# Kernel tuning notes

Hardware: AMD Instinct MI355X
Metric: run time of the kernel (lower is better)

## Reference

```python
import jax, jax.numpy as jnp
import numpy as np

R, N, B, S = 20, 4096, 16, 256          # relations, total nodes, graphs, nodes per graph
DIN, HID, H = 512, 128, 4               # in_dim, hidden_dim, num_heads
D = HID * H                              # flattened node-feature width (=512)
E = 16384                                # edges per relation
NEG_SLOPE = 0.2


def _gat(h, src, dst, W, al, ar, b):
    # DGL GATConv, eval mode (dropout off), identity residual (in == H*out), allow_zero_in_degree
    z = (h @ W).reshape(N, H, HID)                        # [N,H,Dh]
    el = (z * al).sum(-1)                                 # [N,H]
    er = (z * ar).sum(-1)                                 # [N,H]
    e = jax.nn.leaky_relu(el[src] + er[dst], NEG_SLOPE)   # [E,H]
    m = jax.ops.segment_max(e, dst, num_segments=N)       # per-dst max (edge softmax)
    ex = jnp.exp(e - m[dst])
    den = jax.ops.segment_sum(ex, dst, num_segments=N)
    alpha = ex / den[dst]                                 # [E,H]
    agg = jax.ops.segment_sum(alpha[..., None] * z[src], dst, num_segments=N)
    return agg + h.reshape(N, H, HID) + b, alpha


def _rgat_conv(h, src, dst, W, al, ar, b):
    # HeteroGraphConv with aggregate='mean' over R relations; scan keeps memory flat
    def body(acc, xs):
        s, d, Wr, alr, arr, br = xs
        out, alpha = _gat(h, s, d, Wr, alr, arr, br)
        return acc + out, alpha.mean(-1)                  # attention meaned over heads -> [E]
    acc, attn = jax.lax.scan(body, jnp.zeros((N, H, HID), h.dtype), (src, dst, W, al, ar, b))
    return acc / R, attn                                  # [N,H,Dh], [R,E]


def setup_inputs() -> dict:
    key = jax.random.key(0)
    ks = jax.random.split(key, 24)
    f32 = jnp.float32
    p = lambda k, shape: jax.random.normal(k, shape, f32) * 0.05
    z = lambda shape: jnp.zeros(shape, f32)
    return {
        'feat': jax.random.normal(ks[0], (N, DIN), f32),
        'hyp_emb': jax.random.normal(ks[1], (B, D), f32),
        'edge_src': jax.random.randint(ks[2], (R, E), 0, N),
        'edge_dst': jax.random.randint(ks[3], (R, E), 0, N),
        'W1': p(ks[4], (R, DIN, H * HID)), 'al1': p(ks[5], (R, H, HID)), 'ar1': p(ks[6], (R, H, HID)), 'b1': z((R, H, HID)),
        'W2': p(ks[7], (R, D, H * HID)), 'al2': p(ks[8], (R, H, HID)), 'ar2': p(ks[9], (R, H, HID)), 'b2': z((R, H, HID)),
        'Wq': p(ks[10], (D, D)), 'bq': z(D), 'Wk': p(ks[11], (D, D)), 'bk': z(D),
        'Wv': p(ks[12], (D, D)), 'bv': z(D), 'Wo': p(ks[13], (D, D)), 'bo': z(D),
        'Wn1': p(ks[14], (2 * D, HID)), 'bn1': z(HID), 'Wn2': p(ks[15], (HID, 2)), 'bn2': z(2),
    }


def reference(feat, hyp_emb, edge_src, edge_dst,
              W1, al1, ar1, b1, W2, al2, ar2, b2,
              Wq, bq, Wk, bk, Wv, bv, Wo, bo, Wn1, bn1, Wn2, bn2):
    # --- RGAT (rgat_generation) layer 1 + attention weights ---
    h1, attn = _rgat_conv(feat, edge_src, edge_dst, W1, al1, ar1, b1)
    h1 = jax.nn.elu(h1.reshape(N, D))
    # --- layer 2 ---
    h2, _ = _rgat_conv(h1, edge_src, edge_dst, W2, al2, ar2, b2)
    feats = h2.reshape(N, D)
    # --- node importance: scatter-add edge attention onto dst nodes, summed over etypes ---
    imp = jax.ops.segment_sum(attn.reshape(-1), edge_dst.reshape(-1), num_segments=N)
    feats_p = feats.reshape(B, S, D)                      # uniform graphs: split+pad == reshape
    weighted = feats_p * imp.reshape(B, S)[..., None]
    # --- MultiheadAttention(embed=D, heads=4): query = hyp_emb broadcast to all S positions ---
    Hm, Dm = 4, D // 4
    q = (hyp_emb @ Wq + bq).reshape(B, Hm, 1, Dm)         # identical query at every position
    k = (feats_p @ Wk + bk).reshape(B, S, Hm, Dm).transpose(0, 2, 1, 3)
    v = (feats_p @ Wv + bv).reshape(B, S, Hm, Dm).transpose(0, 2, 1, 3)
    scores = jnp.einsum('bhqd,bhkd->bhqk', q, k) / jnp.sqrt(jnp.float32(Dm))
    a = jax.nn.softmax(scores, axis=-1)                   # [B,Hm,1,S]
    ctx = jnp.einsum('bhqk,bhkd->bhqd', a, v).reshape(B, 1, D)
    attn_out = jnp.broadcast_to(ctx @ Wo + bo, (B, S, D))
    # --- node classifier on concat(weighted feats, attention output) ---
    combined = jnp.concatenate([weighted, attn_out], axis=-1).reshape(N, 2 * D)
    node_logits = jax.nn.relu(combined @ Wn1 + bn1) @ Wn2 + bn2
    return node_logits, attn
```

## Files before the change

kernel.cpp:

```cpp
#include <hip/hip_runtime.h>
#include <hip/hip_bf16.h>
#include <math.h>

#define NREL 20
#define NN   4096
#define NE   16384
#define DF   512
#define NHD  4
#define DHH  128
#define NB   16
#define NS   256

typedef __attribute__((ext_vector_type(8))) __bf16 bf16x8;
typedef __attribute__((ext_vector_type(4))) float f32x4;
typedef __attribute__((ext_vector_type(2))) float f32x2;

struct f8 { unsigned char b; };

__device__ inline float bf2f(unsigned short u) {
    union { float f; unsigned int i; } c; c.i = ((unsigned int)u) << 16; return c.f;
}
__device__ inline unsigned short f2bu(float f) {
    union { __hip_bfloat16 b; unsigned short u; } c; c.b = __float2bfloat16(f); return c.u;
}
__device__ inline void storeOut(float* p, float v) { *p = v; }
__device__ inline void storeOut(__hip_bfloat16* p, float v) { *p = __float2bfloat16(v); }

__device__ inline void load_lds16(const __hip_bfloat16* g, __hip_bfloat16* l) {
    __builtin_amdgcn_global_load_lds(
        (const __attribute__((address_space(1))) unsigned int*)(const void*)g,
        (__attribute__((address_space(3))) unsigned int*)(void*)l, 16, 0, 0);
}

__device__ inline int kswz(int f, int row) { return f ^ (((row) & 7) << 3); }

__global__ __launch_bounds__(256) void prep_kernel(
    const float* __restrict__ feat, unsigned short* __restrict__ featbf,
    const float* __restrict__ b1, const float* __restrict__ b2,
    const float* __restrict__ bk, const float* __restrict__ bv,
    float* __restrict__ bsum1, float* __restrict__ bsum2,
    float* __restrict__ bkv, int* __restrict__ cnt, float* __restrict__ imp)
{
    int blk = blockIdx.x, t = threadIdx.x;
    if (blk < 1024) {
        int idx = blk * 256 + t;
        int row = idx >> 6;
        int f = (idx & 63) * 8;
        int fs = kswz(f, row);
        const float4* ip = (const float4*)&feat[(size_t)row * DF + f];
        float4 v0 = ip[0], v1 = ip[1];
        union { unsigned short u[8]; uint4 q; } o;
        o.u[0] = f2bu(v0.x); o.u[1] = f2bu(v0.y); o.u[2] = f2bu(v0.z); o.u[3] = f2bu(v0.w);
        o.u[4] = f2bu(v1.x); o.u[5] = f2bu(v1.y); o.u[6] = f2bu(v1.z); o.u[7] = f2bu(v1.w);
        *(uint4*)(featbf + (size_t)row * DF + fs) = o.q;
    } else if (blk == 1024) {
        #pragma unroll
        for (int rep = 0; rep < 2; ++rep) {
            int f = t + rep * 256;
            float s1 = 0.f, s2 = 0.f;
            #pragma unroll
            for (int r = 0; r < NREL; ++r) { s1 += b1[r * DF + f]; s2 += b2[r * DF + f]; }
            bsum1[f] = s1; bsum2[f] = s2;
        }
        for (int i = t; i < NN; i += 256) imp[i] = 0.f;
    } else if (blk == 1025) {
        #pragma unroll
        for (int j = 0; j < 4; ++j) {
            int f = t + j * 256;
            bkv[f] = (f < DF) ? bk[f] : bv[f - DF];
        }
    } else {
        int idx = (blk - 1026) * 256 + t;
        cnt[idx] = 0;
    }
}

__global__ void count_kernel(const int* __restrict__ dst, int* __restrict__ cnt) {
    int idx = blockIdx.x * 256 + threadIdx.x;
    int r = idx / NE;
    atomicAdd(&cnt[r * NN + dst[idx]], 1);
}

__global__ void scan_kernel(const int* __restrict__ cnt, int* __restrict__ rowptr,
                            int* __restrict__ woff, int* __restrict__ rowptr2,
                            int* __restrict__ croff) {
    int r = blockIdx.x;
    int t = threadIdx.x;
    __shared__ int sums[1024];
    int v[4]; int local = 0;
    if (r < NREL) {
        #pragma unroll
        for (int j = 0; j < 4; ++j) { v[j] = cnt[r * NN + t * 4 + j]; local += v[j]; }
    } else {
        #pragma unroll
        for (int j = 0; j < 4; ++j) {
            int s = 0;
            for (int rel = 0; rel < NREL; ++rel) {
                croff[rel * NN + t * 4 + j] = s;
                s += cnt[rel * NN + t * 4 + j];
            }
            v[j] = s; local += s;
        }
    }
    sums[t] = local;
    __syncthreads();
    for (int off = 1; off < 1024; off <<= 1) {
        int x = (t >= off) ? sums[t - off] : 0;
        __syncthreads();
        sums[t] += x;
        __syncthreads();
    }
    int run = (t == 0) ? 0 : sums[t - 1];
    if (r < NREL) {
        #pragma unroll
        for (int j = 0; j < 4; ++j) {
            rowptr[r * (NN + 1) + t * 4 + j] = run;
            woff[r * NN + t * 4 + j] = run;
            run += v[j];
        }
        if (t == 1023) rowptr[r * (NN + 1) + NN] = run;
    } else {
        #pragma unroll
        for (int j = 0; j < 4; ++j) { rowptr2[t * 4 + j] = run; run += v[j]; }
        if (t == 1023) rowptr2[NN] = run;
    }
}

__global__ void fill_kernel(const int* __restrict__ dst, const int* __restrict__ src,
                            int* __restrict__ woff, int* __restrict__ srcCSR,
                            int* __restrict__ eidCSR) {
    int idx = blockIdx.x * 256 + threadIdx.x;
    int r = idx / NE; int e = idx % NE;
    int pos = atomicAdd(&woff[r * NN + dst[idx]], 1);
    srcCSR[r * NE + pos] = src[idx];
    eidCSR[r * NE + pos] = e;
}

__global__ __launch_bounds__(256) void transw_kernel(
    const float* __restrict__ W, __hip_bfloat16* __restrict__ Wt, int K, int N)
{
    int r = blockIdx.z;
    __shared__ float t[32][33];
    int k0 = blockIdx.x * 32, n0 = blockIdx.y * 32;
    int tx = threadIdx.x % 32, ty = threadIdx.x / 32;
    #pragma unroll
    for (int kk = ty; kk < 32; kk += 8)
        t[kk][tx] = W[((size_t)r * K + k0 + kk) * N + n0 + tx];
    __syncthreads();
    #pragma unroll
    for (int nn = ty; nn < 32; nn += 8) {
        int row = n0 + nn;
        Wt[((size_t)r * N + row) * K + kswz(k0 + tx, row)] = __float2bfloat16(t[tx][nn]);
    }
}

__global__ __launch_bounds__(256) void transw2_kernel(
    const float* __restrict__ W1, const float* __restrict__ W2,
    const float* __restrict__ Wk, const float* __restrict__ Wv,
    __hip_bfloat16* __restrict__ Wt1, __hip_bfloat16* __restrict__ Wt2,
    __hip_bfloat16* __restrict__ WtKV)
{
    int z = blockIdx.z;
    const float* Wsrc; __hip_bfloat16* Wdst;
    if (z < NREL)           { Wsrc = W1 + (size_t)z * DF * DF;          Wdst = Wt1 + (size_t)z * DF * DF; }
    else if (z < 2 * NREL)  { Wsrc = W2 + (size_t)(z - NREL) * DF * DF; Wdst = Wt2 + (size_t)(z - NREL) * DF * DF; }
    else if (z == 2 * NREL) { Wsrc = Wk;                                Wdst = WtKV; }
    else                    { Wsrc = Wv;                                Wdst = WtKV + (size_t)DF * DF; }
    __shared__ float t[32][33];
    int k0 = blockIdx.x * 32, n0 = blockIdx.y * 32;
    int tx = threadIdx.x % 32, ty = threadIdx.x / 32;
    #pragma unroll
    for (int kk = ty; kk < 32; kk += 8)
        t[kk][tx] = Wsrc[(size_t)(k0 + kk) * DF + n0 + tx];
    __syncthreads();
    #pragma unroll
    for (int nn = ty; nn < 32; nn += 8) {
        int row = n0 + nn;
        Wdst[(size_t)row * DF + kswz(k0 + tx, row)] = __float2bfloat16(t[tx][nn]);
    }
}

__global__ __launch_bounds__(512) void zgemm8(
    const __hip_bfloat16* __restrict__ A,
    const __hip_bfloat16* __restrict__ BtAll,
    unsigned char* __restrict__ Zall,
    const float* __restrict__ al, const float* __restrict__ ar,
    float* __restrict__ el, float* __restrict__ er)
{
    const int r = blockIdx.z;
    const __hip_bfloat16* Bt = BtAll + (size_t)r * DF * DF;
    unsigned char* Z = Zall + (size_t)r * NN * DF;
    const int rowBase = blockIdx.y * 256;
    const int colBase = blockIdx.x * 256;
    __shared__ __hip_bfloat16 As[2][256][64];
    __shared__ __hip_bfloat16 Bs[2][256][64];
    const int tid = threadIdx.x;
    const int w = tid >> 6, l = tid & 63;
    const int wr = w >> 2, wc = w & 3;
    const int m15 = l & 15, q = l >> 4;
    const int swr = m15 & 7;

    const __hip_bfloat16* Ag = A + (size_t)(rowBase + (tid >> 3)) * DF + (tid & 7) * 8;
    const __hip_bfloat16* Bg = Bt + (size_t)(colBase + (tid >> 3)) * DF + (tid & 7) * 8;
    __hip_bfloat16* AsT = &As[0][0][0] + tid * 8;
    __hip_bfloat16* BsT = &Bs[0][0][0] + tid * 8;

#define STAGE_A(buf, half, kt) do { \
        const __hip_bfloat16* s_ = Ag + (size_t)((half) * 128) * DF + (kt) * 64; \
        __hip_bfloat16* d_ = AsT + (buf) * 16384 + (half) * 8192; \
        load_lds16(s_, d_); \
        load_lds16(s_ + (size_t)64 * DF, d_ + 4096); } while (0)
#define STAGE_B(buf, half, kt) do { \
        const __hip_bfloat16* s_ = Bg + (size_t)((half) * 128) * DF + (kt) * 64; \
        __hip_bfloat16* d_ = BsT + (buf) * 16384 + (half) * 8192; \
        load_lds16(s_, d_); \
        load_lds16(s_ + (size_t)64 * DF, d_ + 4096); } while (0)

    f32x4 acc[8][4];
    #pragma unroll
    for (int i = 0; i < 8; ++i)
        #pragma unroll
        for (int j = 0; j < 4; ++j) acc[i][j] = (f32x4){0.f, 0.f, 0.f, 0.f};

    const int NT = DF / 64;
    STAGE_A(0, 0, 0); STAGE_A(0, 1, 0); STAGE_B(0, 0, 0); STAGE_B(0, 1, 0);
    STAGE_A(1, 0, 1); STAGE_A(1, 1, 1); STAGE_B(1, 0, 1); STAGE_B(1, 1, 1);
    asm volatile("s_waitcnt vmcnt(8)" ::: "memory");
    __builtin_amdgcn_s_barrier();
    __builtin_amdgcn_sched_barrier(0);

    bf16x8 a0[8], a1[8], b0[4], b1[4];
    for (int kt = 0; kt < NT; ++kt) {
        const int buf = kt & 1;
        #pragma unroll
        for (int i = 0; i < 8; ++i) {
            a0[i] = *(const bf16x8*)&As[buf][wr * 128 + i * 16 + m15][(q ^ swr) * 8];
            a1[i] = *(const bf16x8*)&As[buf][wr * 128 + i * 16 + m15][((4 + q) ^ swr) * 8];
        }
        #pragma unroll
        for (int j = 0; j < 4; ++j) {
            b0[j] = *(const bf16x8*)&Bs[buf][wc * 64 + j * 16 + m15][(q ^ swr) * 8];
            b1[j] = *(const bf16x8*)&Bs[buf][wc * 64 + j * 16 + m15][((4 + q) ^ swr) * 8];
        }
        asm volatile("s_waitcnt lgkmcnt(0)" ::: "memory");
        __builtin_amdgcn_s_barrier();
        __builtin_amdgcn_sched_barrier(0);
        if (kt + 2 < NT) {
            STAGE_A(buf, 0, kt + 2); STAGE_A(buf, 1, kt + 2);
            STAGE_B(buf, 0, kt + 2); STAGE_B(buf, 1, kt + 2);
        }
        __builtin_amdgcn_s_setprio(1);
        #pragma unroll
        for (int i = 0; i < 8; ++i)
            #pragma unroll
            for (int j = 0; j < 4; ++j)
                acc[i][j] = __builtin_amdgcn_mfma_f32_16x16x32_bf16(a0[i], b0[j], acc[i][j], 0, 0, 0);
        #pragma unroll
        for (int i = 0; i < 8; ++i)
            #pragma unroll
            for (int j = 0; j < 4; ++j)
                acc[i][j] = __builtin_amdgcn_mfma_f32_16x16x32_bf16(a1[i], b1[j], acc[i][j], 0, 0, 0);
        __builtin_amdgcn_s_setprio(0);
        if (kt + 2 < NT)      { asm volatile("s_waitcnt vmcnt(8)" ::: "memory"); }
        else if (kt + 1 < NT) { asm volatile("s_waitcnt vmcnt(0)" ::: "memory"); }
        __builtin_amdgcn_s_barrier();
        __builtin_amdgcn_sched_barrier(0);
    }
#undef STAGE_A
#undef STAGE_B

    unsigned char* cbuf = (unsigned char*)&As[0][0][0];
    #pragma unroll
    for (int i = 0; i < 8; ++i)
        #pragma unroll
        for (int j = 0; j < 4; ++j) {
            int colL = wc * 64 + j * 16 + m15;
            #pragma unroll
            for (int reg = 0; reg < 4; ++reg) {
                int rowL = wr * 128 + i * 16 + q * 4 + reg;
                unsigned int pk = __builtin_amdgcn_cvt_pk_fp8_f32(
                    acc[i][j][reg], acc[i][j][reg], 0, false);
                cbuf[rowL * 256 + colL] = (unsigned char)(pk & 0xFF);
            }
        }
    __syncthreads();
    {
        int rowL = tid >> 1, colL = (tid & 1) * 128;
        const uint4* src = (const uint4*)&cbuf[rowL * 256 + colL];
        uint4* dst = (uint4*)(Z + (size_t)(rowBase + rowL) * DF + colBase + colL);
        #pragma unroll
        for (int x = 0; x < 8; ++x) dst[x] = src[x];
    }

    float alv[4], arv[4];
    #pragma unroll
    for (int j = 0; j < 4; ++j) {
        int col = colBase + wc * 64 + j * 16 + m15;
        alv[j] = al[r * DF + col];
        arv[j] = ar[r * DF + col];
    }
    float pe[8][4], pr[8][4];
    #pragma unroll
    for (int i = 0; i < 8; ++i)
        #pragma unroll
        for (int reg = 0; reg < 4; ++reg) {
            float se = 0.f, sr = 0.f;
            #pragma unroll
            for (int j = 0; j < 4; ++j) {
                se += acc[i][j][reg] * alv[j];
                sr += acc[i][j][reg] * arv[j];
            }
            pe[i][reg] = se; pr[i][reg] = sr;
        }
    #pragma unroll
    for (int off = 1; off < 16; off <<= 1)
        #pragma unroll
        for (int i = 0; i < 8; ++i)
            #pragma unroll
            for (int reg = 0; reg < 4; ++reg) {
                pe[i][reg] += __shfl_xor(pe[i][reg], off);
                pr[i][reg] += __shfl_xor(pr[i][reg], off);
            }
    float* eP = (float*)&Bs[0][0][0];
    float* rP = eP + 1024;
    if (m15 == 0) {
        int hh = wc >> 1, strip = wc & 1;
        #pragma unroll
        for (int i = 0; i < 8; ++i)
            #pragma unroll
            for (int reg = 0; reg < 4; ++reg) {
                int rowL = wr * 128 + i * 16 + q * 4 + reg;
                eP[(hh * 256 + rowL) * 2 + strip] = pe[i][reg];
                rP[(hh * 256 + rowL) * 2 + strip] = pr[i][reg];
            }
    }
    __syncthreads();
    {
        int rowL = tid & 255, hh = tid >> 8;
        int head = (colBase >> 7) + hh;
        size_t idx = ((size_t)r * NN + rowBase + rowL) * NHD + head;
        el[idx] = eP[(hh * 256 + rowL) * 2] + eP[(hh * 256 + rowL) * 2 + 1];
        er[idx] = rP[(hh * 256 + rowL) * 2] + rP[(hh * 256 + rowL) * 2 + 1];
    }
}

template <typename OutT, bool RELU, bool FUSE, bool SPLITK = false>
__global__ __launch_bounds__(256) void mfma_gemm(
    const __hip_bfloat16* __restrict__ A,
    const __hip_bfloat16* __restrict__ BtAll,
    const float* __restrict__ bias, int biasStride,
    OutT* __restrict__ Call, int M, int N, int K, int lda,
    const float* __restrict__ al, const float* __restrict__ ar,
    float* __restrict__ el, float* __restrict__ er)
{
    int r = blockIdx.z;
    const __hip_bfloat16* Bt;
    int koff;
    if (SPLITK) { Bt = BtAll;                         koff = r * K; }
    else        { Bt = BtAll + (size_t)r * N * lda;   koff = 0; }
    OutT* C = Call + (size_t)r * M * N;
    const int rowBase = blockIdx.y * 128;
    const int colBase = blockIdx.x * 128;
    __shared__ __hip_bfloat16 As[128 * 64];
    __shared__ __hip_bfloat16 Bs[128 * 64];
    const int tid = threadIdx.x;
    const int w = tid >> 6, l = tid & 63;
    const int wr = w >> 1, wc = w & 1;
    const int m15 = l & 15, q = l >> 4;
    const int sRow = tid >> 3;
    const int sChk = tid & 7;
    const __hip_bfloat16* Ag = A + (size_t)(rowBase + sRow) * lda + koff + sChk * 8;
    const __hip_bfloat16* Bg = Bt + (size_t)(colBase + sRow) * lda + koff + sChk * 8;
    __hip_bfloat16* Asl = As + tid * 8;
    __hip_bfloat16* Bsl = Bs + tid * 8;
    const int swr = m15 & 7;

    f32x4 acc[4][4];
    #pragma unroll
    for (int i = 0; i < 4; ++i)
        #pragma unroll
        for (int j = 0; j < 4; ++j) acc[i][j] = (f32x4){0.f, 0.f, 0.f, 0.f};

    for (int k0 = 0; k0 < K; k0 += 64) {
        #pragma unroll
        for (int c = 0; c < 4; ++c) {
            load_lds16(Ag + (size_t)c * 32 * lda + k0, Asl + c * 2048);
            load_lds16(Bg + (size_t)c * 32 * lda + k0, Bsl + c * 2048);
        }
        __syncthreads();
        #pragma unroll
        for (int g = 0; g < 2; ++g) {
            bf16x8 a[4], b[4];
            #pragma unroll
            for (int i = 0; i < 4; ++i)
                a[i] = *(const bf16x8*)&As[(wr * 64 + i * 16 + m15) * 64 + ((g * 4 + q) ^ swr) * 8];
            #pragma unroll
            for (int j = 0; j < 4; ++j)
                b[j] = *(const bf16x8*)&Bs[(wc * 64 + j * 16 + m15) * 64 + ((g * 4 + q) ^ swr) * 8];
            #pragma unroll
            for (int i = 0; i < 4; ++i)
                #pragma unroll
                for (int j = 0; j < 4; ++j)
                    acc[i][j] = __builtin_amdgcn_mfma_f32_16x16x32_bf16(a[i], b[j], acc[i][j], 0, 0, 0);
        }
        __syncthreads();
    }

    if constexpr (sizeof(OutT) == 1) {
        unsigned char* cbuf = (unsigned char*)As;
        #pragma unroll
        for (int i = 0; i < 4; ++i)
            #pragma unroll
            for (int j = 0; j < 4; ++j) {
                int colL = wc * 64 + j * 16 + m15;
                #pragma unroll
                for (int reg = 0; reg < 4; ++reg) {
                    int rowL = wr * 64 + i * 16 + q * 4 + reg;
                    unsigned int pk = __builtin_amdgcn_cvt_pk_fp8_f32(
                        acc[i][j][reg], acc[i][j][reg], 0, false);
                    cbuf[rowL * 128 + colL] = (unsigned char)(pk & 0xFF);
                }
            }
        __syncthreads();
        int rowL = tid >> 1, colL = (tid & 1) * 64;
        const uint4* src = (const uint4*)&cbuf[rowL * 128 + colL];
        uint4* dst = (uint4*)((unsigned char*)C + (size_t)(rowBase + rowL) * N
                              + colBase + colL);
        #pragma unroll
        for (int x = 0; x < 4; ++x) dst[x] = src[x];
    } else {
        #pragma unroll
        for (int i = 0; i < 4; ++i) {
            #pragma unroll
            for (int j = 0; j < 4; ++j) {
                int col = colBase + wc * 64 + j * 16 + m15;
                float bv = bias ? bias[r * biasStride + col] : 0.f;
                #pragma unroll
                for (int reg = 0; reg < 4; ++reg) {
                    int row = rowBase + wr * 64 + i * 16 + q * 4 + reg;
                    float v = acc[i][j][reg] + bv;
                    if (RELU) v = fmaxf(v, 0.f);
                    storeOut(&C[(size_t)row * N + col], v);
                }
            }
        }
    }

    if (FUSE) {
        float alv[4], arv[4];
        #pragma unroll
        for (int j = 0; j < 4; ++j) {
            int col = colBase + wc * 64 + j * 16 + m15;
            alv[j] = al[r * DF + col];
            arv[j] = ar[r * DF + col];
        }
        float pe[4][4], pr[4][4];
        #pragma unroll
        for (int i = 0; i < 4; ++i)
            #pragma unroll
            for (int reg = 0; reg < 4; ++reg) {
                float se = 0.f, sr = 0.f;
                #pragma unroll
                for (int j = 0; j < 4; ++j) {
                    se += acc[i][j][reg] * alv[j];
                    sr += acc[i][j][reg] * arv[j];
                }
                pe[i][reg] = se; pr[i][reg] = sr;
            }
        #pragma unroll
        for (int off = 1; off < 16; off <<= 1)
            #pragma unroll
            for (int i = 0; i < 4; ++i)
                #pragma unroll
                for (int reg = 0; reg < 4; ++reg) {
                    pe[i][reg] += __shfl_xor(pe[i][reg], off);
                    pr[i][reg] += __shfl_xor(pr[i][reg], off);
                }
        float* eP = (float*)Bs;
        float* rP = eP + 256;
        if (m15 == 0) {
            #pragma unroll
            for (int i = 0; i < 4; ++i)
                #pragma unroll
                for (int reg = 0; reg < 4; ++reg) {
                    int rowL = wr * 64 + i * 16 + q * 4 + reg;
                    eP[rowL * 2 + wc] = pe[i][reg];
                    rP[rowL * 2 + wc] = pr[i][reg];
                }
        }
        __syncthreads();
        if (tid < 128) {
            int head = colBase >> 7;
            size_t idx = ((size_t)r * NN + rowBase + tid) * NHD + head;
            el[idx] = eP[tid * 2] + eP[tid * 2 + 1];
            er[idx] = rP[tid * 2] + rP[tid * 2 + 1];
        }
    }
}

template <typename OutT>
__global__ __launch_bounds__(256) void gemm_kernel(
    const float* __restrict__ A, const float* __restrict__ Bm,
    const float* __restrict__ bias, OutT* __restrict__ C,
    int M, int K, int Nn)
{
    int r = blockIdx.z;
    const float* B = Bm + (size_t)r * K * Nn;
    OutT* Cr = C + (size_t)r * M * Nn;
    int rowBase = blockIdx.y * 64;
    int colBase = blockIdx.x * 64;
    __shared__ float As[64][17];
    __shared__ float Bs[16][64];
    int tid = threadIdx.x;
    int tx = tid % 16, ty = tid / 16;
    float acc[4][4] = {};
    int aRow = tid / 4, aK4 = (tid % 4) * 4;
    int bK = tid / 16, bN4 = (tid % 16) * 4;
    for (int k0 = 0; k0 < K; k0 += 16) {
        int gRow = rowBase + aRow;
        float4 av = make_float4(0.f, 0.f, 0.f, 0.f);
        if (gRow < M) av = *(const float4*)(A + (size_t)gRow * K + k0 + aK4);
        As[aRow][aK4 + 0] = av.x; As[aRow][aK4 + 1] = av.y;
        As[aRow][aK4 + 2] = av.z; As[aRow][aK4 + 3] = av.w;
        float4 bv = *(const float4*)(B + (size_t)(k0 + bK) * Nn + colBase + bN4);
        *(float4*)&Bs[bK][bN4] = bv;
        __syncthreads();
        #pragma unroll
        for (int k = 0; k < 16; ++k) {
            float a[4], b[4];
            #pragma unroll
            for (int i = 0; i < 4; ++i) a[i] = As[ty * 4 + i][k];
            #pragma unroll
            for (int j = 0; j < 4; ++j) b[j] = Bs[k][tx * 4 + j];
            #pragma unroll
            for (int i = 0; i < 4; ++i)
                #pragma unroll
                for (int j = 0; j < 4; ++j) acc[i][j] += a[i] * b[j];
        }
        __syncthreads();
    }
    #pragma unroll
    for (int i = 0; i < 4; ++i) {
        int gRow = rowBase + ty * 4 + i;
        if (gRow >= M) continue;
        #pragma unroll
        for (int j = 0; j < 4; ++j) {
            int gCol = colBase + tx * 4 + j;
            float v = acc[i][j];
            if (bias) v += bias[gCol];
            storeOut(&Cr[(size_t)gRow * Nn + gCol], v);
        }
    }
}

__global__ __launch_bounds__(256) void alpha_kernel(
    const float* __restrict__ el, const float* __restrict__ er,
    const int* __restrict__ rowptr, const int* __restrict__ rowptr2,
    const int* __restrict__ croff, const int* __restrict__ srcCSR,
    const int* __restrict__ eidCSR,
    float* __restrict__ alphaPk, int* __restrict__ srcPk,
    float* __restrict__ attn, float* __restrict__ imp)
{
    int t = blockIdx.x * 256 + threadIdx.x;
    int r = t / NN, n = t % NN;
    int start = rowptr[r * (NN + 1) + n];
    int d = rowptr[r * (NN + 1) + n + 1] - start;
    if (d == 0) return;
    int pbase = rowptr2[n] + croff[r * NN + n];
    float4 er4 = *(const float4*)&er[((size_t)r * NN + n) * NHD];
    float4 den = make_float4(0.f, 0.f, 0.f, 0.f);
    for (int j = 0; j < d; ++j) {
        int s = srcCSR[r * NE + start + j];
        float4 el4 = *(const float4*)&el[((size_t)r * NN + s) * NHD];
        float v0 = el4.x + er4.x; v0 = v0 > 0.f ? v0 : 0.2f * v0;
        float v1 = el4.y + er4.y; v1 = v1 > 0.f ? v1 : 0.2f * v1;
        float v2 = el4.z + er4.z; v2 = v2 > 0.f ? v2 : 0.2f * v2;
        float v3 = el4.w + er4.w; v3 = v3 > 0.f ? v3 : 0.2f * v3;
        float4 e4 = make_float4(__expf(v0), __expf(v1), __expf(v2), __expf(v3));
        den.x += e4.x; den.y += e4.y; den.z += e4.z; den.w += e4.w;
        *(float4*)&alphaPk[(size_t)(pbase + j) * 4] = e4;
        srcPk[pbase + j] = r * NN + s;
    }
    float4 inv = make_float4(1.f / den.x, 1.f / den.y, 1.f / den.z, 1.f / den.w);
    float impLoc = 0.f;
    for (int j = 0; j < d; ++j) {
        float4 a4 = *(const float4*)&alphaPk[(size_t)(pbase + j) * 4];
        a4.x *= inv.x; a4.y *= inv.y; a4.z *= inv.z; a4.w *= inv.w;
        *(float4*)&alphaPk[(size_t)(pbase + j) * 4] = a4;
        if (attn) {
            float a = 0.25f * (a4.x + a4.y + a4.z + a4.w);
            attn[r * NE + eidCSR[r * NE + start + j]] = a;
            impLoc += a;
        }
    }
    if (attn) atomicAdd(&imp[n], impLoc);
}

__global__ __launch_bounds__(256) void aggc_kernel(
    const unsigned char* __restrict__ Z,
    const int* __restrict__ rowptr2, const int* __restrict__ srcPk,
    const float* __restrict__ alphaPk, const float* __restrict__ bsum,
    const float* __restrict__ hin, float* __restrict__ hout,
    __hip_bfloat16* __restrict__ hout_bf, int applyElu)
{
    int n = blockIdx.x;
    int w = threadIdx.x >> 6, lane = threadIdx.x & 63;
    int h = lane >> 4;
    int base = rowptr2[n];
    int deg = rowptr2[n + 1] - base;
    float acc[8] = {};
    if (deg > 0) {
        int i = w * 4;
        int zz[4]; float aa[4];
        #pragma unroll
        for (int j = 0; j < 4; ++j) {
            int idx = i + j; int cidx = idx < deg ? idx : deg - 1;
            zz[j] = srcPk[base + cidx];
            aa[j] = (idx < deg) ? alphaPk[(size_t)(base + cidx) * 4 + h] : 0.f;
        }
        while (i < deg) {
            int cz[4]; float ca[4];
            #pragma unroll
            for (int j = 0; j < 4; ++j) { cz[j] = zz[j]; ca[j] = aa[j]; }
            int ni = i + 16;
            #pragma unroll
            for (int j = 0; j < 4; ++j) {
                int idx = ni + j; int cidx = idx < deg ? idx : deg - 1;
                zz[j] = srcPk[base + cidx];
                aa[j] = (idx < deg) ? alphaPk[(size_t)(base + cidx) * 4 + h] : 0.f;
            }
            uint2 raw[4];
            #pragma unroll
            for (int j = 0; j < 4; ++j)
                raw[j] = *(const uint2*)&Z[(size_t)cz[j] * DF + lane * 8];
            #pragma unroll
            for (int j = 0; j < 4; ++j) {
                f32x2 f01 = __builtin_amdgcn_cvt_pk_f32_fp8((int)raw[j].x, false);
                f32x2 f23 = __builtin_amdgcn_cvt_pk_f32_fp8((int)raw[j].x, true);
                f32x2 f45 = __builtin_amdgcn_cvt_pk_f32_fp8((int)raw[j].y, false);
                f32x2 f67 = __builtin_amdgcn_cvt_pk_f32_fp8((int)raw[j].y, true);
                acc[0] += ca[j] * f01.x; acc[1] += ca[j] * f01.y;
                acc[2] += ca[j] * f23.x; acc[3] += ca[j] * f23.y;
                acc[4] += ca[j] * f45.x; acc[5] += ca[j] * f45.y;
                acc[6] += ca[j] * f67.x; acc[7] += ca[j] * f67.y;
            }
            i = ni;
        }
    }
    __shared__ float red[4][DF];
    #pragma unroll
    for (int j = 0; j < 8; ++j) red[w][lane * 8 + j] = acc[j];
    __syncthreads();
    const float invR = 1.0f / NREL;
    const int sw = (n & 7) << 3;
    int f = threadIdx.x;
    #pragma unroll
    for (int rep = 0; rep < 2; ++rep, f += 256) {
        float v = red[0][f] + red[1][f] + red[2][f] + red[3][f];
        v = (v + bsum[f]) * invR + hin[(size_t)n * DF + f];
        if (applyElu) v = v > 0.f ? v : expm1f(v);
        hout[(size_t)n * DF + f] = v;
        hout_bf[(size_t)n * DF + (f ^ sw)] = __float2bfloat16(v);
    }
}

__global__ __launch_bounds__(256) void mha_scores(
    const float* __restrict__ q, const float* __restrict__ k,
    float* __restrict__ scores)
{
    int b = blockIdx.x;
    int w = threadIdx.x >> 6, lane = threadIdx.x & 63;
    int s = blockIdx.y * 4 + w;
    const float4* qp = (const float4*)&q[(size_t)b * DF + lane * 8];
    const float4* kp = (const float4*)&k[((size_t)(b * NS + s)) * DF + lane * 8];
    float4 q0 = qp[0], q1 = qp[1];
    float4 k0 = kp[0], k1 = kp[1];
    float p = q0.x * k0.x + q0.y * k0.y + q0.z * k0.z + q0.w * k0.w
            + q1.x * k1.x + q1.y * k1.y + q1.z * k1.z + q1.w * k1.w;
    #pragma unroll
    for (int off = 1; off < 16; off <<= 1) p += __shfl_xor(p, off);
    if ((lane & 15) == 0) {
        int h = lane >> 4;
        scores[((size_t)(b * NHD + h)) * NS + s] = p * 0.08838834764831845f;
    }
}

__global__ __launch_bounds__(256) void mha_ctx(
    const float* __restrict__ scores, const float* __restrict__ v,
    float* __restrict__ ctx)
{
    int b = blockIdx.x, h = blockIdx.y;
    int t = threadIdx.x;
    int lane = t & 63, w = t >> 6;
    __shared__ float a_s[NS];
    __shared__ float wred[8];
    float sv = scores[((size_t)(b * NHD + h)) * NS + t];
    float mx = sv;
    #pragma unroll
    for (int off = 1; off < 64; off <<= 1) mx = fmaxf(mx, __shfl_xor(mx, off));
    if (lane == 0) wred[w] = mx;
    __syncthreads();
    mx = fmaxf(fmaxf(wred[0], wred[1]), fmaxf(wred[2], wred[3]));
    float e = __expf(sv - mx);
    float sum = e;
    #pragma unroll
    for (int off = 1; off < 64; off <<= 1) sum += __shfl_xor(sum, off);
    if (lane == 0) wred[4 + w] = sum;
    __syncthreads();
    sum = wred[4] + wred[5] + wred[6] + wred[7];
    a_s[t] = e * (1.0f / sum);
    __syncthreads();
    int d = t & 127, half = t >> 7;
    float acc = 0.f;
    const float* vp = &v[((size_t)(b * NS + half * 128)) * DF + h * DHH + d];
    #pragma unroll 4
    for (int i = 0; i < 128; ++i)
        acc += a_s[half * 128 + i] * vp[(size_t)i * DF];
    __shared__ float red[256];
    red[t] = acc;
    __syncthreads();
    if (t < 128) ctx[(size_t)b * DF + h * DHH + t] = red[t] + red[t + 128];
}

__global__ __launch_bounds__(256) void combined_kernel(
    const float* __restrict__ feats, const float* __restrict__ imp,
    const float* __restrict__ abuf, __hip_bfloat16* __restrict__ comb)
{
    int n = blockIdx.x;
    int t = threadIdx.x;
    int b = n >> 8;
    float im = imp[n];
    const int sw = (n & 7) << 3;
    #pragma unroll
    for (int rep = 0; rep < 4; ++rep) {
        int f = t + rep * 256;
        float v = (f < DF) ? feats[(size_t)n * DF + f] * im
                           : abuf[(size_t)b * DF + (f - DF)];
        comb[(size_t)n * (2 * DF) + (f ^ sw)] = __float2bfloat16(v);
    }
}

__global__ __launch_bounds__(256) void cls2_kernel(
    const float* __restrict__ hidden4, const float* __restrict__ bn1,
    const float* __restrict__ Wn2, const float* __restrict__ bn2,
    float* __restrict__ out)
{
    __shared__ float w2[256];
    __shared__ float b1s[128];
    int t = threadIdx.x;
    w2[t] = Wn2[t];
    if (t < 128) b1s[t] = bn1[t];
    __syncthreads();
    int n = blockIdx.x * 256 + t;
    const float* hp = &hidden4[(size_t)n * 128];
    const size_t ps = (size_t)NN * 128;
    float p0 = bn2[0], p1 = bn2[1];
    #pragma unroll 4
    for (int kk = 0; kk < 128; ++kk) {
        float hv = hp[kk] + hp[ps + kk] + hp[2 * ps + kk] + hp[3 * ps + kk] + b1s[kk];
        hv = fmaxf(hv, 0.f);
        p0 += hv * w2[kk * 2 + 0];
        p1 += hv * w2[kk * 2 + 1];
    }
    out[n * 2 + 0] = p0;
    out[n * 2 + 1] = p1;
}

extern "C" void kernel_launch(void* const* d_in, const int* in_sizes, int n_in,
                              void* d_out, int out_size, void* d_ws, size_t ws_size,
                              hipStream_t stream) {
    const float* feat = (const float*)d_in[0];
    const float* hyp  = (const float*)d_in[1];
    const int*   esrc = (const int*)d_in[2];
    const int*   edst = (const int*)d_in[3];
    const float* W1   = (const float*)d_in[4];
    const float* al1  = (const float*)d_in[5];
    const float* ar1  = (const float*)d_in[6];
    const float* b1   = (const float*)d_in[7];
    const float* W2   = (const float*)d_in[8];
    const float* al2  = (const float*)d_in[9];
    const float* ar2  = (const float*)d_in[10];
    const float* b2   = (const float*)d_in[11];
    const float* Wq = (const float*)d_in[12]; const float* bq = (const float*)d_in[13];
    const float* Wk = (const float*)d_in[14]; const float* bk = (const float*)d_in[15];
    const float* Wv = (const float*)d_in[16]; const float* bv = (const float*)d_in[17];
    const float* Wo = (const float*)d_in[18]; const float* bo = (const float*)d_in[19];
    const float* Wn1 = (const float*)d_in[20]; const float* bn1 = (const float*)d_in[21];
    const float* Wn2 = (const float*)d_in[22]; const float* bn2 = (const float*)d_in[23];

    char* ws = (char*)d_ws;
    size_t off = 0;
    auto alloc = [&](size_t bytes) -> void* {
        void* p = ws + off;
        off += (bytes + 255) & ~(size_t)255;
        return p;
    };
    unsigned char* Z = (unsigned char*)alloc((size_t)NREL * NN * DF);
    float* el     = (float*)alloc((size_t)NREL * NN * NHD * 4);
    float* er     = (float*)alloc((size_t)NREL * NN * NHD * 4);
    int* rowptr   = (int*)alloc((size_t)NREL * (NN + 1) * 4);
    int* rowptr2  = (int*)alloc((size_t)(NN + 1) * 4);
    int* woff     = (int*)alloc((size_t)NREL * NN * 4);
    int* srcCSR   = (int*)alloc((size_t)NREL * NE * 4);
    int* eidCSR   = (int*)alloc((size_t)NREL * NE * 4);
    int* cnt      = (int*)alloc((size_t)NREL * NN * 4);
    int* croff    = (int*)alloc((size_t)NREL * NN * 4);
    int* srcPk    = (int*)alloc((size_t)NREL * NE * 4);
    float* alphaPk= (float*)alloc((size_t)NREL * NE * NHD * 4);
    float* bsum1  = (float*)alloc((size_t)DF * 4);
    float* bsum2  = (float*)alloc((size_t)DF * 4);
    float* bkv    = (float*)alloc((size_t)2 * DF * 4);
    float* h1     = (float*)alloc((size_t)NN * DF * 4);
    float* feats  = (float*)alloc((size_t)NN * DF * 4);
    float* imp    = (float*)alloc((size_t)NN * 4);
    float* kvbuf  = (float*)alloc((size_t)2 * NN * DF * 4);
    float* qbuf   = (float*)alloc((size_t)NB * DF * 4);
    float* ctxb   = (float*)alloc((size_t)NB * DF * 4);
    float* abuf   = (float*)alloc((size_t)NB * DF * 4);
    float* scoresb= (float*)alloc((size_t)NB * NHD * NS * 4);
    float* hidden4= (float*)alloc((size_t)4 * NN * 128 * 4);
    __hip_bfloat16* featbf  = (__hip_bfloat16*)alloc((size_t)NN * DF * 2);
    __hip_bfloat16* h1bf    = (__hip_bfloat16*)alloc((size_t)NN * DF * 2);
    __hip_bfloat16* featsbf = (__hip_bfloat16*)alloc((size_t)NN * DF * 2);
    __hip_bfloat16* combbf  = (__hip_bfloat16*)alloc((size_t)NN * 2 * DF * 2);
    __hip_bfloat16* Wt1 = (__hip_bfloat16*)alloc((size_t)NREL * DF * DF * 2);
    __hip_bfloat16* Wt2 = (__hip_bfloat16*)alloc((size_t)NREL * DF * DF * 2);
    __hip_bfloat16* WtKV = (__hip_bfloat16*)alloc((size_t)2 * DF * DF * 2);
    __hip_bfloat16* Wn1t = (__hip_bfloat16*)alloc((size_t)(2 * DF) * 128 * 2);
    if (off > ws_size) return;

    float* logits = (float*)d_out;
    float* attn   = (float*)d_out + (size_t)NN * 2;
    float* kbuf = kvbuf;
    float* vbuf = kvbuf + (size_t)NN * DF;

    prep_kernel<<<1026 + NREL * NN / 256, 256, 0, stream>>>(
        feat, (unsigned short*)featbf, b1, b2, bk, bv, bsum1, bsum2, bkv, cnt, imp);

    count_kernel<<<NREL * NE / 256, 256, 0, stream>>>(edst, cnt);
    scan_kernel<<<NREL + 1, 1024, 0, stream>>>(cnt, rowptr, woff, rowptr2, croff);
    fill_kernel<<<NREL * NE / 256, 256, 0, stream>>>(edst, esrc, woff, srcCSR, eidCSR);

    transw2_kernel<<<dim3(DF / 32, DF / 32, 2 * NREL + 2), 256, 0, stream>>>(
        W1, W2, Wk, Wv, Wt1, Wt2, WtKV);
    transw_kernel<<<dim3(2 * DF / 32, 128 / 32, 1), 256, 0, stream>>>(Wn1, Wn1t, 2 * DF, 128);

    zgemm8<<<dim3(DF / 256, NN / 256, NREL), 512, 0, stream>>>(
        featbf, Wt1, Z, al1, ar1, el, er);
    alpha_kernel<<<NREL * NN / 256, 256, 0, stream>>>(
        el, er, rowptr, rowptr2, croff, srcCSR, eidCSR, alphaPk, srcPk, attn, imp);
    aggc_kernel<<<NN, 256, 0, stream>>>(Z, rowptr2, srcPk, alphaPk, bsum1,
                                        feat, h1, h1bf, 1);

    zgemm8<<<dim3(DF / 256, NN / 256, NREL), 512, 0, stream>>>(
        h1bf, Wt2, Z, al2, ar2, el, er);
    alpha_kernel<<<NREL * NN / 256, 256, 0, stream>>>(
        el, er, rowptr, rowptr2, croff, srcCSR, eidCSR, alphaPk, srcPk, nullptr, nullptr);
    aggc_kernel<<<NN, 256, 0, stream>>>(Z, rowptr2, srcPk, alphaPk, bsum2,
                                        h1, feats, featsbf, 0);

    mfma_gemm<float, false, false><<<dim3(DF / 128, NN / 128, 2), 256, 0, stream>>>(
        featsbf, WtKV, bkv, DF, kvbuf, NN, DF, DF, DF, nullptr, nullptr, nullptr, nullptr);
    gemm_kernel<float><<<dim3(DF / 64, 1, 1), 256, 0, stream>>>(
        hyp, Wq, bq, qbuf, NB, DF, DF);
    mha_scores<<<dim3(NB, NS / 4), 256, 0, stream>>>(qbuf, kbuf, scoresb);
    mha_ctx<<<dim3(NB, NHD), 256, 0, stream>>>(scoresb, vbuf, ctxb);
    gemm_kernel<float><<<dim3(DF / 64, 1, 1), 256, 0, stream>>>(
        ctxb, Wo, bo, abuf, NB, DF, DF);

    combined_kernel<<<NN, 256, 0, stream>>>(feats, imp, abuf, combbf);
    mfma_gemm<float, false, false, true><<<dim3(1, NN / 128, 4), 256, 0, stream>>>(
        combbf, Wn1t, nullptr, 0, hidden4, NN, 128, 256, 2 * DF,
        nullptr, nullptr, nullptr, nullptr);
    cls2_kernel<<<NN / 256, 256, 0, stream>>>(hidden4, bn1, Wn2, bn2, logits);
}
```

Before: 582.8 us.

## Fuse MHA query, scores, softmax, context and output projection into one kernel

Four small kernels (Q projection GEMM, scores, softmax plus context, output projection GEMM) are replaced by a single per-batch kernel that keeps the intermediates in shared memory, removing launch overhead and global round trips. Separately, the zgemm8 main loop is reordered so the first half-K MFMAs start after only the first LDS fragments arrive, overlapping the second-half LDS reads with compute. The fused kernel runs only 16 blocks and does serial 512-long dot products per thread, so the projection stages may be latency-bound in exchange.

Result: no change. 588.3 us (+0.9%).

```diff
diff --git a/kernel.cpp b/kernel.cpp
--- a/kernel.cpp
+++ b/kernel.cpp
@@ -233,28 +233,37 @@
     for (int kt = 0; kt < NT; ++kt) {
         const int buf = kt & 1;
         #pragma unroll
-        for (int i = 0; i < 8; ++i) {
+        for (int i = 0; i < 8; ++i)
             a0[i] = *(const bf16x8*)&As[buf][wr * 128 + i * 16 + m15][(q ^ swr) * 8];
+        #pragma unroll
+        for (int j = 0; j < 4; ++j)
+            b0[j] = *(const bf16x8*)&Bs[buf][wc * 64 + j * 16 + m15][(q ^ swr) * 8];
+        asm volatile("s_waitcnt lgkmcnt(0)" ::: "memory");
+        __builtin_amdgcn_sched_barrier(0);
+        #pragma unroll
+        for (int i = 0; i < 8; ++i)
             a1[i] = *(const bf16x8*)&As[buf][wr * 128 + i * 16 + m15][((4 + q) ^ swr) * 8];
-        }
-        #pragma unroll
-        for (int j = 0; j < 4; ++j) {
-            b0[j] = *(const bf16x8*)&Bs[buf][wc * 64 + j * 16 + m15][(q ^ swr) * 8];
+        #pragma unroll
+        for (int j = 0; j < 4; ++j)
             b1[j] = *(const bf16x8*)&Bs[buf][wc * 64 + j * 16 + m15][((4 + q) ^ swr) * 8];
-        }
+        __builtin_amdgcn_sched_barrier(0);
+        __builtin_amdgcn_s_setprio(1);
+        #pragma unroll
+        for (int i = 0; i < 8; ++i)
+            #pragma unroll
+            for (int j = 0; j < 4; ++j)
+                acc[i][j] = __builtin_amdgcn_mfma_f32_16x16x32_bf16(a0[i], b0[j], acc[i][j], 0, 0, 0);
+        __builtin_amdgcn_s_setprio(0);
         asm volatile("s_waitcnt lgkmcnt(0)" ::: "memory");
+        __builtin_amdgcn_sched_barrier(0);
         __builtin_amdgcn_s_barrier();
         __builtin_amdgcn_sched_barrier(0);
         if (kt + 2 < NT) {
             STAGE_A(buf, 0, kt + 2); STAGE_A(buf, 1, kt + 2);
             STAGE_B(buf, 0, kt + 2); STAGE_B(buf, 1, kt + 2);
         }
+        __builtin_amdgcn_sched_barrier(0);
         __builtin_amdgcn_s_setprio(1);
-        #pragma unroll
-        for (int i = 0; i < 8; ++i)
-            #pragma unroll
-            for (int j = 0; j < 4; ++j)
-                acc[i][j] = __builtin_amdgcn_mfma_f32_16x16x32_bf16(a0[i], b0[j], acc[i][j], 0, 0, 0);
         #pragma unroll
         for (int i = 0; i < 8; ++i)
             #pragma unroll
@@ -498,61 +507,6 @@
     }
 }
 
-template <typename OutT>
-__global__ __launch_bounds__(256) void gemm_kernel(
-    const float* __restrict__ A, const float* __restrict__ Bm,
-    const float* __restrict__ bias, OutT* __restrict__ C,
-    int M, int K, int Nn)
-{
-    int r = blockIdx.z;
-    const float* B = Bm + (size_t)r * K * Nn;
-    OutT* Cr = C + (size_t)r * M * Nn;
-    int rowBase = blockIdx.y * 64;
-    int colBase = blockIdx.x * 64;
-    __shared__ float As[64][17];
-    __shared__ float Bs[16][64];
-    int tid = threadIdx.x;
-    int tx = tid % 16, ty = tid / 16;
-    float acc[4][4] = {};
-    int aRow = tid / 4, aK4 = (tid % 4) * 4;
-    int bK = tid / 16, bN4 = (tid % 16) * 4;
-    for (int k0 = 0; k0 < K; k0 += 16) {
-        int gRow = rowBase + aRow;
-        float4 av = make_float4(0.f, 0.f, 0.f, 0.f);
-        if (gRow < M) av = *(const float4*)(A + (size_t)gRow * K + k0 + aK4);
-        As[aRow][aK4 + 0] = av.x; As[aRow][aK4 + 1] = av.y;
-        As[aRow][aK4 + 2] = av.z; As[aRow][aK4 + 3] = av.w;
-        float4 bv = *(const float4*)(B + (size_t)(k0 + bK) * Nn + colBase + bN4);
-        *(float4*)&Bs[bK][bN4] = bv;
-        __syncthreads();
-        #pragma unroll
-        for (int k = 0; k < 16; ++k) {
-            float a[4], b[4];
-            #pragma unroll
-            for (int i = 0; i < 4; ++i) a[i] = As[ty * 4 + i][k];
-            #pragma unroll
-            for (int j = 0; j < 4; ++j) b[j] = Bs[k][tx * 4 + j];
-            #pragma unroll
-            for (int i = 0; i < 4; ++i)
-                #pragma unroll
-                for (int j = 0; j < 4; ++j) acc[i][j] += a[i] * b[j];
-        }
-        __syncthreads();
-    }
-    #pragma unroll
-    for (int i = 0; i < 4; ++i) {
-        int gRow = rowBase + ty * 4 + i;
-        if (gRow >= M) continue;
-        #pragma unroll
-        for (int j = 0; j < 4; ++j) {
-            int gCol = colBase + tx * 4 + j;
-            float v = acc[i][j];
-            if (bias) v += bias[gCol];
-            storeOut(&Cr[(size_t)gRow * Nn + gCol], v);
-        }
-    }
-}
-
 __global__ __launch_bounds__(256) void alpha_kernel(
     const float* __restrict__ el, const float* __restrict__ er,
     const int* __restrict__ rowptr, const int* __restrict__ rowptr2,
@@ -664,62 +618,86 @@
     }
 }
 
-__global__ __launch_bounds__(256) void mha_scores(
-    const float* __restrict__ q, const float* __restrict__ k,
-    float* __restrict__ scores)
-{
-    int b = blockIdx.x;
-    int w = threadIdx.x >> 6, lane = threadIdx.x & 63;
-    int s = blockIdx.y * 4 + w;
-    const float4* qp = (const float4*)&q[(size_t)b * DF + lane * 8];
-    const float4* kp = (const float4*)&k[((size_t)(b * NS + s)) * DF + lane * 8];
-    float4 q0 = qp[0], q1 = qp[1];
-    float4 k0 = kp[0], k1 = kp[1];
-    float p = q0.x * k0.x + q0.y * k0.y + q0.z * k0.z + q0.w * k0.w
-            + q1.x * k1.x + q1.y * k1.y + q1.z * k1.z + q1.w * k1.w;
-    #pragma unroll
-    for (int off = 1; off < 16; off <<= 1) p += __shfl_xor(p, off);
-    if ((lane & 15) == 0) {
-        int h = lane >> 4;
-        scores[((size_t)(b * NHD + h)) * NS + s] = p * 0.08838834764831845f;
-    }
-}
-
-__global__ __launch_bounds__(256) void mha_ctx(
-    const float* __restrict__ scores, const float* __restrict__ v,
-    float* __restrict__ ctx)
-{
-    int b = blockIdx.x, h = blockIdx.y;
-    int t = threadIdx.x;
-    int lane = t & 63, w = t >> 6;
-    __shared__ float a_s[NS];
-    __shared__ float wred[8];
-    float sv = scores[((size_t)(b * NHD + h)) * NS + t];
-    float mx = sv;
-    #pragma unroll
-    for (int off = 1; off < 64; off <<= 1) mx = fmaxf(mx, __shfl_xor(mx, off));
-    if (lane == 0) wred[w] = mx;
-    __syncthreads();
-    mx = fmaxf(fmaxf(wred[0], wred[1]), fmaxf(wred[2], wred[3]));
-    float e = __expf(sv - mx);
-    float sum = e;
-    #pragma unroll
-    for (int off = 1; off < 64; off <<= 1) sum += __shfl_xor(sum, off);
-    if (lane == 0) wred[4 + w] = sum;
-    __syncthreads();
-    sum = wred[4] + wred[5] + wred[6] + wred[7];
-    a_s[t] = e * (1.0f / sum);
-    __syncthreads();
-    int d = t & 127, half = t >> 7;
-    float acc = 0.f;
-    const float* vp = &v[((size_t)(b * NS + half * 128)) * DF + h * DHH + d];
-    #pragma unroll 4
-    for (int i = 0; i < 128; ++i)
-        acc += a_s[half * 128 + i] * vp[(size_t)i * DF];
-    __shared__ float red[256];
-    red[t] = acc;
-    __syncthreads();
-    if (t < 128) ctx[(size_t)b * DF + h * DHH + t] = red[t] + red[t + 128];
+__global__ __launch_bounds__(256) void mha_fused(
+    const float* __restrict__ hyp, const float* __restrict__ Wq,
+    const float* __restrict__ bq, const float* __restrict__ kv,
+    const float* __restrict__ Wo, const float* __restrict__ bo,
+    float* __restrict__ abuf)
+{
+    const int b = blockIdx.x, t = threadIdx.x;
+    const int w = t >> 6, lane = t & 63;
+    __shared__ float hq[DF];
+    __shared__ float qv[DF];
+    __shared__ float sc[NHD][NS];
+    __shared__ float cx[DF];
+    hq[t] = hyp[(size_t)b * DF + t];
+    hq[t + 256] = hyp[(size_t)b * DF + t + 256];
+    __syncthreads();
+    {
+        float a0 = bq[t], a1 = bq[t + 256];
+        for (int k = 0; k < DF; ++k) {
+            float hv = hq[k];
+            a0 += hv * Wq[(size_t)k * DF + t];
+            a1 += hv * Wq[(size_t)k * DF + t + 256];
+        }
+        qv[t] = a0; qv[t + 256] = a1;
+    }
+    __syncthreads();
+    {
+        const float4* qp = (const float4*)&qv[lane * 8];
+        float4 q0 = qp[0], q1 = qp[1];
+        for (int s = w; s < NS; s += 4) {
+            const float4* kp = (const float4*)&kv[((size_t)(b * NS + s)) * DF + lane * 8];
+            float4 k0 = kp[0], k1 = kp[1];
+            float p = q0.x * k0.x + q0.y * k0.y + q0.z * k0.z + q0.w * k0.w
+                    + q1.x * k1.x + q1.y * k1.y + q1.z * k1.z + q1.w * k1.w;
+            #pragma unroll
+            for (int off = 1; off < 16; off <<= 1) p += __shfl_xor(p, off);
+            if ((lane & 15) == 0)
+                sc[lane >> 4][s] = p * 0.08838834764831845f;
+        }
+    }
+    __syncthreads();
+    {
+        float v4[4];
+        float mx = -INFINITY;
+        #pragma unroll
+        for (int i = 0; i < 4; ++i) { v4[i] = sc[w][lane + 64 * i]; mx = fmaxf(mx, v4[i]); }
+        #pragma unroll
+        for (int off = 32; off; off >>= 1) mx = fmaxf(mx, __shfl_xor(mx, off));
+        float sum = 0.f;
+        #pragma unroll
+        for (int i = 0; i < 4; ++i) { v4[i] = __expf(v4[i] - mx); sum += v4[i]; }
+        #pragma unroll
+        for (int off = 32; off; off >>= 1) sum += __shfl_xor(sum, off);
+        float inv = 1.0f / sum;
+        #pragma unroll
+        for (int i = 0; i < 4; ++i) sc[w][lane + 64 * i] = v4[i] * inv;
+    }
+    __syncthreads();
+    {
+        int h = t >> 7, d = t & 127;
+        int h2 = h + 2;
+        float c0 = 0.f, c1 = 0.f;
+        for (int s = 0; s < NS; ++s) {
+            const float* vp = &kv[((size_t)(NN + b * NS + s)) * DF];
+            c0 += sc[h][s]  * vp[h * DHH + d];
+            c1 += sc[h2][s] * vp[h2 * DHH + d];
+        }
+        cx[h * DHH + d] = c0;
+        cx[h2 * DHH + d] = c1;
+    }
+    __syncthreads();
+    {
+        float o0 = bo[t], o1 = bo[t + 256];
+        for (int k = 0; k < DF; ++k) {
+            float cv = cx[k];
+            o0 += cv * Wo[(size_t)k * DF + t];
+            o1 += cv * Wo[(size_t)k * DF + t + 256];
+        }
+        abuf[(size_t)b * DF + t] = o0;
+        abuf[(size_t)b * DF + t + 256] = o1;
+    }
 }
 
 __global__ __launch_bounds__(256) void combined_kernel(
@@ -814,10 +792,7 @@
     float* feats  = (float*)alloc((size_t)NN * DF * 4);
     float* imp    = (float*)alloc((size_t)NN * 4);
     float* kvbuf  = (float*)alloc((size_t)2 * NN * DF * 4);
-    float* qbuf   = (float*)alloc((size_t)NB * DF * 4);
-    float* ctxb   = (float*)alloc((size_t)NB * DF * 4);
     float* abuf   = (float*)alloc((size_t)NB * DF * 4);
-    float* scoresb= (float*)alloc((size_t)NB * NHD * NS * 4);
     float* hidden4= (float*)alloc((size_t)4 * NN * 128 * 4);
     __hip_bfloat16* featbf  = (__hip_bfloat16*)alloc((size_t)NN * DF * 2);
     __hip_bfloat16* h1bf    = (__hip_bfloat16*)alloc((size_t)NN * DF * 2);
@@ -832,7 +807,6 @@
     float* logits = (float*)d_out;
     float* attn   = (float*)d_out + (size_t)NN * 2;
     float* kbuf = kvbuf;
-    float* vbuf = kvbuf + (size_t)NN * DF;
 
     prep_kernel<<<1026 + NREL * NN / 256, 256, 0, stream>>>(
         feat, (unsigned short*)featbf, b1, b2, bk, bv, bsum1, bsum2, bkv, cnt, imp);
@@ -861,12 +835,7 @@
 
     mfma_gemm<float, false, false><<<dim3(DF / 128, NN / 128, 2), 256, 0, stream>>>(
         featsbf, WtKV, bkv, DF, kvbuf, NN, DF, DF, DF, nullptr, nullptr, nullptr, nullptr);
-    gemm_kernel<float><<<dim3(DF / 64, 1, 1), 256, 0, stream>>>(
-        hyp, Wq, bq, qbuf, NB, DF, DF);
-    mha_scores<<<dim3(NB, NS / 4), 256, 0, stream>>>(qbuf, kbuf, scoresb);
-    mha_ctx<<<dim3(NB, NHD), 256, 0, stream>>>(scoresb, vbuf, ctxb);
-    gemm_kernel<float><<<dim3(DF / 64, 1, 1), 256, 0, stream>>>(
-        ctxb, Wo, bo, abuf, NB, DF, DF);
+    mha_fused<<<NB, 256, 0, stream>>>(hyp, Wq, bq, kbuf, Wo, bo, abuf);
 
     combined_kernel<<<NN, 256, 0, stream>>>(feats, imp, abuf, combbf);
     mfma_gemm<float, false, false, true><<<dim3(1, NN / 128, 4), 256, 0, stream>>>(
```
